# Optimization experiments

Hardware: AMD Instinct MI355X
Metric: run time of the kernel (lower is better)

## Reference

```python
import jax, jax.numpy as jnp
import numpy as np

EMB_DIM = 512          # hidden_dim d (complex dim); entity rows are 2*d
NUM_ENTITIES = 30000
GAMMA = 12.0
PHASE_RANGE = (GAMMA + 2.0) / EMB_DIM  # self.range in the torch module


def setup_inputs() -> dict:
    key = jax.random.key(0)
    k1, k2, k3, k4 = jax.random.split(key, 4)
    B = 8
    all_h = jax.random.randint(k1, (B,), 0, NUM_ENTITIES, dtype=jnp.int64 if jax.config.x64_enabled else jnp.int32)
    all_r = jax.random.randint(k2, (B,), 0, 1000, dtype=jnp.int64 if jax.config.x64_enabled else jnp.int32)
    eemb = jax.random.normal(k3, (NUM_ENTITIES, 2 * EMB_DIM), dtype=jnp.float32)
    remb = jax.random.normal(k4, (1000, EMB_DIM), dtype=jnp.float32)
    return {"all_h": all_h, "all_r": all_r, "eemb": eemb, "remb": remb}


def reference(all_h, all_r, eemb, remb):
    pi = 3.141592653589793
    # gather query embeddings
    h = eemb[all_h]                       # (B, 2d)
    re_h, im_h = jnp.split(h, 2, axis=-1)  # (B, d) each
    # project relation phases -> unit complex rotation
    phase = remb[all_r] / (PHASE_RANGE / pi)  # (B, d)
    re_r, im_r = jnp.cos(phase), jnp.sin(phase)
    # complex product h * r (rotation), once per query
    re_e = re_h * re_r - im_h * im_r      # (B, d)
    im_e = re_h * im_r + im_h * re_r      # (B, d)
    # distance to ALL entities: |h*r - t| summed over complex components
    re_t, im_t = jnp.split(eemb, 2, axis=-1)  # (N, d) each
    re_diff = re_e[:, None, :] - re_t[None, :, :]  # (B, N, d)
    im_diff = im_e[:, None, :] - im_t[None, :, :]  # (B, N, d)
    dist = jnp.sqrt(re_diff * re_diff + im_diff * im_diff).sum(axis=-1)  # (B, N)
    return GAMMA - dist
```

## Files before the change

### kernel.cpp

```cpp
#include <hip/hip_runtime.h>
#include <math.h>

#define EMB_DIM 512
#define N_Q 8
#define GAMMA_F 12.0f

typedef float f32x4 __attribute__((ext_vector_type(4)));

__global__ __launch_bounds__(256) void rotate_queries_kernel(
    const int* __restrict__ all_h,
    const int* __restrict__ all_r,
    const float* __restrict__ eemb,
    const float* __restrict__ remb,
    float* __restrict__ ws)
{
    const int p = blockIdx.x * 256 + threadIdx.x;
    const int b = p >> 9;
    const int j = p & (EMB_DIM - 1);
    const int h = all_h[b];
    const int r = all_r[b];
    const float SCALE = (float)(M_PI * (double)EMB_DIM / 14.0);
    float re_h = eemb[(size_t)h * (2 * EMB_DIM) + j];
    float im_h = eemb[(size_t)h * (2 * EMB_DIM) + EMB_DIM + j];
    float phase = remb[r * EMB_DIM + j] * SCALE;
    float s, c;
    __sincosf(phase, &s, &c);
    ws[p]                 = re_h * c - im_h * s;
    ws[N_Q * EMB_DIM + p] = re_h * s + im_h * c;
}

__global__ __launch_bounds__(256, 2) void rotate_score_kernel(
    const float* __restrict__ eemb,
    const float* __restrict__ ws,
    float* __restrict__ out,
    int N)
{
    const int lane  = threadIdx.x & 63;
    const int wid   = threadIdx.x >> 6;
    const int gwave = blockIdx.x * 4 + wid;
    const int nwav  = gridDim.x * 4;

    const int o0 = 4 * lane;
    const int o1 = 256 + 4 * lane;

    f32x4 qr0[N_Q], qr1[N_Q], qi0[N_Q], qi1[N_Q];
    #pragma unroll
    for (int b = 0; b < N_Q; ++b) {
        const float* re = ws + (b << 9);
        const float* im = re + N_Q * EMB_DIM;
        qr0[b] = *(const f32x4*)(re + o0);
        qr1[b] = *(const f32x4*)(re + o1);
        qi0[b] = *(const f32x4*)(im + o0);
        qi1[b] = *(const f32x4*)(im + o1);
    }

    int e = gwave;
    const float* rp = eemb + (size_t)e * (2 * EMB_DIM);
    f32x4 er0 = *(const f32x4*)(rp + o0);
    f32x4 er1 = *(const f32x4*)(rp + o1);
    f32x4 ei0 = *(const f32x4*)(rp + EMB_DIM + o0);
    f32x4 ei1 = *(const f32x4*)(rp + EMB_DIM + o1);

    for (; e < N; e += nwav) {
        int en = e + nwav;
        int ec = (en < N) ? en : 0;
        const float* np = eemb + (size_t)ec * (2 * EMB_DIM);
        f32x4 nr0 = *(const f32x4*)(np + o0);
        f32x4 nr1 = *(const f32x4*)(np + o1);
        f32x4 ni0 = *(const f32x4*)(np + EMB_DIM + o0);
        f32x4 ni1 = *(const f32x4*)(np + EMB_DIM + o1);

        float s[N_Q];
        #pragma unroll
        for (int b = 0; b < N_Q; ++b) {
            f32x4 dx = qr0[b] - er0;
            f32x4 dy = qi0[b] - ei0;
            f32x4 d2 = dx * dx + dy * dy;
            f32x4 ra;
            ra.x = __builtin_amdgcn_sqrtf(d2.x);
            ra.y = __builtin_amdgcn_sqrtf(d2.y);
            ra.z = __builtin_amdgcn_sqrtf(d2.z);
            ra.w = __builtin_amdgcn_sqrtf(d2.w);
            dx = qr1[b] - er1;
            dy = qi1[b] - ei1;
            d2 = dx * dx + dy * dy;
            f32x4 rb;
            rb.x = __builtin_amdgcn_sqrtf(d2.x);
            rb.y = __builtin_amdgcn_sqrtf(d2.y);
            rb.z = __builtin_amdgcn_sqrtf(d2.z);
            rb.w = __builtin_amdgcn_sqrtf(d2.w);
            f32x4 a = ra + rb;
            s[b] = (a.x + a.y) + (a.z + a.w);
        }

        const bool p1 = lane & 1;
        float u0, u1, u2, u3;
        {
            float x, z;
            x = p1 ? s[1] : s[0]; z = p1 ? s[0] : s[1]; u0 = x + __shfl_xor(z, 1);
            x = p1 ? s[3] : s[2]; z = p1 ? s[2] : s[3]; u1 = x + __shfl_xor(z, 1);
            x = p1 ? s[5] : s[4]; z = p1 ? s[4] : s[5]; u2 = x + __shfl_xor(z, 1);
            x = p1 ? s[7] : s[6]; z = p1 ? s[6] : s[7]; u3 = x + __shfl_xor(z, 1);
        }
        const bool p2 = lane & 2;
        float t0, t1;
        {
            float x, z;
            x = p2 ? u1 : u0; z = p2 ? u0 : u1; t0 = x + __shfl_xor(z, 2);
            x = p2 ? u3 : u2; z = p2 ? u2 : u3; t1 = x + __shfl_xor(z, 2);
        }
        const bool p3 = lane & 4;
        float u;
        {
            float x, z;
            x = p3 ? t1 : t0; z = p3 ? t0 : t1; u = x + __shfl_xor(z, 4);
        }
        u += __shfl_xor(u, 8);
        u += __shfl_xor(u, 16);
        u += __shfl_xor(u, 32);

        if (lane < N_Q) out[(size_t)lane * N + e] = GAMMA_F - u;

        er0 = nr0; er1 = nr1; ei0 = ni0; ei1 = ni1;
    }
}

extern "C" void kernel_launch(void* const* d_in, const int* in_sizes, int n_in,
                              void* d_out, int out_size, void* d_ws, size_t ws_size,
                              hipStream_t stream) {
    const int*   all_h = (const int*)d_in[0];
    const int*   all_r = (const int*)d_in[1];
    const float* eemb  = (const float*)d_in[2];
    const float* remb  = (const float*)d_in[3];
    float* out = (float*)d_out;
    float* ws  = (float*)d_ws;

    int N = in_sizes[2] / (2 * EMB_DIM);

    rotate_queries_kernel<<<16, 256, 0, stream>>>(all_h, all_r, eemb, remb, ws);

    rotate_score_kernel<<<512, 256, 0, stream>>>(eemb, ws, out, N);
}
```

Before: 184.8 us.

## Fuse query rotation into score kernel, split queries across waves, triple-buffer loads

Removes the separate query-rotation launch by having each wave compute its own rotated queries inline. Each wave now handles 4 of the 8 queries, so two waves share each entity row and the entity stream is read twice, but register pressure drops. This allows 3 blocks per CU and a larger grid of 768 blocks. The entity loads now use a three-deep rotating register buffer so loads run further ahead of the sqrt-heavy compute. The cost is doubled entity loads, which will mostly hit L2, plus redundant sincos work in every wave.

```diff
diff --git a/kernel.cpp b/kernel.cpp
--- a/kernel.cpp
+++ b/kernel.cpp
@@ -7,121 +7,137 @@
 
 typedef float f32x4 __attribute__((ext_vector_type(4)));
 
-__global__ __launch_bounds__(256) void rotate_queries_kernel(
+
+#define LOADE(R0, R1, I0, I1, EIDX)                                   \
+    do {                                                              \
+        int _ec = ((EIDX) < N) ? (EIDX) : 0;                          \
+        const float* _p = eemb + (size_t)_ec * (2 * EMB_DIM);         \
+        R0 = *(const f32x4*)(_p + o0);                                \
+        R1 = *(const f32x4*)(_p + o1);                                \
+        I0 = *(const f32x4*)(_p + EMB_DIM + o0);                      \
+        I1 = *(const f32x4*)(_p + EMB_DIM + o1);                      \
+    } while (0)
+
+#define SCORE(R0, R1, I0, I1, EIDX)                                   \
+    do {                                                              \
+        float s_[4];                                                  \
+        _Pragma("unroll")                                             \
+        for (int k = 0; k < 4; ++k) {                                 \
+            f32x4 dx = qr0[k] - R0;                                   \
+            f32x4 dy = qi0[k] - I0;                                   \
+            f32x4 d2 = dx * dx + dy * dy;                             \
+            f32x4 ra;                                                 \
+            ra.x = __builtin_amdgcn_sqrtf(d2.x);                      \
+            ra.y = __builtin_amdgcn_sqrtf(d2.y);                      \
+            ra.z = __builtin_amdgcn_sqrtf(d2.z);                      \
+            ra.w = __builtin_amdgcn_sqrtf(d2.w);                      \
+            dx = qr1[k] - R1;                                         \
+            dy = qi1[k] - I1;                                         \
+            d2 = dx * dx + dy * dy;                                   \
+            f32x4 rb;                                                 \
+            rb.x = __builtin_amdgcn_sqrtf(d2.x);                      \
+            rb.y = __builtin_amdgcn_sqrtf(d2.y);                      \
+            rb.z = __builtin_amdgcn_sqrtf(d2.z);                      \
+            rb.w = __builtin_amdgcn_sqrtf(d2.w);                      \
+            f32x4 a = ra + rb;                                        \
+            s_[k] = (a.x + a.y) + (a.z + a.w);                        \
+        }                                                             \
+        const bool p1 = lane & 1;                                     \
+        float x_, z_, u0, u1;                                         \
+        x_ = p1 ? s_[1] : s_[0]; z_ = p1 ? s_[0] : s_[1];             \
+        u0 = x_ + __shfl_xor(z_, 1);                                  \
+        x_ = p1 ? s_[3] : s_[2]; z_ = p1 ? s_[2] : s_[3];             \
+        u1 = x_ + __shfl_xor(z_, 1);                                  \
+        const bool p2 = lane & 2;                                     \
+        x_ = p2 ? u1 : u0; z_ = p2 ? u0 : u1;                         \
+        float u = x_ + __shfl_xor(z_, 2);                             \
+        u += __shfl_xor(u, 4);                                        \
+        u += __shfl_xor(u, 8);                                        \
+        u += __shfl_xor(u, 16);                                       \
+        u += __shfl_xor(u, 32);                                       \
+        if (lane < 4 && (EIDX) < N)                                   \
+            out[(size_t)(qh * 4 + lane) * N + (EIDX)] = GAMMA_F - u;  \
+    } while (0)
+
+__global__ __launch_bounds__(256, 3) void rotate_score_kernel(
     const int* __restrict__ all_h,
     const int* __restrict__ all_r,
     const float* __restrict__ eemb,
     const float* __restrict__ remb,
-    float* __restrict__ ws)
-{
-    const int p = blockIdx.x * 256 + threadIdx.x;
-    const int b = p >> 9;
-    const int j = p & (EMB_DIM - 1);
-    const int h = all_h[b];
-    const int r = all_r[b];
-    const float SCALE = (float)(M_PI * (double)EMB_DIM / 14.0);
-    float re_h = eemb[(size_t)h * (2 * EMB_DIM) + j];
-    float im_h = eemb[(size_t)h * (2 * EMB_DIM) + EMB_DIM + j];
-    float phase = remb[r * EMB_DIM + j] * SCALE;
-    float s, c;
-    __sincosf(phase, &s, &c);
-    ws[p]                 = re_h * c - im_h * s;
-    ws[N_Q * EMB_DIM + p] = re_h * s + im_h * c;
-}
-
-__global__ __launch_bounds__(256, 2) void rotate_score_kernel(
-    const float* __restrict__ eemb,
-    const float* __restrict__ ws,
     float* __restrict__ out,
     int N)
 {
     const int lane  = threadIdx.x & 63;
     const int wid   = threadIdx.x >> 6;
     const int gwave = blockIdx.x * 4 + wid;
-    const int nwav  = gridDim.x * 4;
+    const int W     = gridDim.x * 4;
+    const int qh    = gwave & 1;
+    const int e0    = gwave >> 1;
+    const int estep = W >> 1;
 
     const int o0 = 4 * lane;
     const int o1 = 256 + 4 * lane;
 
-    f32x4 qr0[N_Q], qr1[N_Q], qi0[N_Q], qi1[N_Q];
-    #pragma unroll
-    for (int b = 0; b < N_Q; ++b) {
-        const float* re = ws + (b << 9);
-        const float* im = re + N_Q * EMB_DIM;
-        qr0[b] = *(const f32x4*)(re + o0);
-        qr1[b] = *(const f32x4*)(re + o1);
-        qi0[b] = *(const f32x4*)(im + o0);
-        qi1[b] = *(const f32x4*)(im + o1);
+    f32x4 qr0[4], qr1[4], qi0[4], qi1[4];
+    {
+        const float SCALE = (float)(M_PI * (double)EMB_DIM / 14.0);
+        #pragma unroll
+        for (int k = 0; k < 4; ++k) {
+            int q = qh * 4 + k;
+            int h = all_h[q];
+            int r = all_r[q];
+            const float* hp = eemb + (size_t)h * (2 * EMB_DIM);
+            const float* rp = remb + (size_t)r * EMB_DIM;
+            f32x4 reh0 = *(const f32x4*)(hp + o0);
+            f32x4 reh1 = *(const f32x4*)(hp + o1);
+            f32x4 imh0 = *(const f32x4*)(hp + EMB_DIM + o0);
+            f32x4 imh1 = *(const f32x4*)(hp + EMB_DIM + o1);
+            f32x4 ph0  = *(const f32x4*)(rp + o0);
+            f32x4 ph1  = *(const f32x4*)(rp + o1);
+            f32x4 s0, c0, s1, c1;
+            #pragma unroll
+            for (int j = 0; j < 4; ++j) {
+                float s, c;
+                __sincosf(ph0[j] * SCALE, &s, &c);
+                s0[j] = s; c0[j] = c;
+                __sincosf(ph1[j] * SCALE, &s, &c);
+                s1[j] = s; c1[j] = c;
+            }
+            qr0[k] = reh0 * c0 - imh0 * s0;
+            qr1[k] = reh1 * c1 - imh1 * s1;
+            qi0[k] = reh0 * s0 + imh0 * c0;
+            qi1[k] = reh1 * s1 + imh1 * c1;
+        }
     }
 
-    int e = gwave;
-    const float* rp = eemb + (size_t)e * (2 * EMB_DIM);
-    f32x4 er0 = *(const f32x4*)(rp + o0);
-    f32x4 er1 = *(const f32x4*)(rp + o1);
-    f32x4 ei0 = *(const f32x4*)(rp + EMB_DIM + o0);
-    f32x4 ei1 = *(const f32x4*)(rp + EMB_DIM + o1);
+    f32x4 Ar0, Ar1, Ai0, Ai1;
+    f32x4 Br0, Br1, Bi0, Bi1;
+    f32x4 Cr0, Cr1, Ci0, Ci1;
 
-    for (; e < N; e += nwav) {
-        int en = e + nwav;
-        int ec = (en < N) ? en : 0;
-        const float* np = eemb + (size_t)ec * (2 * EMB_DIM);
-        f32x4 nr0 = *(const f32x4*)(np + o0);
-        f32x4 nr1 = *(const f32x4*)(np + o1);
-        f32x4 ni0 = *(const f32x4*)(np + EMB_DIM + o0);
-        f32x4 ni1 = *(const f32x4*)(np + EMB_DIM + o1);
+    const int itmax = (N + estep - 1) / estep;
+    int e = e0;
+    LOADE(Ar0, Ar1, Ai0, Ai1, e);
+    LOADE(Br0, Br1, Bi0, Bi1, e + estep);
 
-        float s[N_Q];
-        #pragma unroll
-        for (int b = 0; b < N_Q; ++b) {
-            f32x4 dx = qr0[b] - er0;
-            f32x4 dy = qi0[b] - ei0;
-            f32x4 d2 = dx * dx + dy * dy;
-            f32x4 ra;
-            ra.x = __builtin_amdgcn_sqrtf(d2.x);
-            ra.y = __builtin_amdgcn_sqrtf(d2.y);
-            ra.z = __builtin_amdgcn_sqrtf(d2.z);
-            ra.w = __builtin_amdgcn_sqrtf(d2.w);
-            dx = qr1[b] - er1;
-            dy = qi1[b] - ei1;
-            d2 = dx * dx + dy * dy;
-            f32x4 rb;
-            rb.x = __builtin_amdgcn_sqrtf(d2.x);
-            rb.y = __builtin_amdgcn_sqrtf(d2.y);
-            rb.z = __builtin_amdgcn_sqrtf(d2.z);
-            rb.w = __builtin_amdgcn_sqrtf(d2.w);
-            f32x4 a = ra + rb;
-            s[b] = (a.x + a.y) + (a.z + a.w);
-        }
-
-        const bool p1 = lane & 1;
-        float u0, u1, u2, u3;
-        {
-            float x, z;
-            x = p1 ? s[1] : s[0]; z = p1 ? s[0] : s[1]; u0 = x + __shfl_xor(z, 1);
-            x = p1 ? s[3] : s[2]; z = p1 ? s[2] : s[3]; u1 = x + __shfl_xor(z, 1);
-            x = p1 ? s[5] : s[4]; z = p1 ? s[4] : s[5]; u2 = x + __shfl_xor(z, 1);
-            x = p1 ? s[7] : s[6]; z = p1 ? s[6] : s[7]; u3 = x + __shfl_xor(z, 1);
-        }
-        const bool p2 = lane & 2;
-        float t0, t1;
-        {
-            float x, z;
-            x = p2 ? u1 : u0; z = p2 ? u0 : u1; t0 = x + __shfl_xor(z, 2);
-            x = p2 ? u3 : u2; z = p2 ? u2 : u3; t1 = x + __shfl_xor(z, 2);
-        }
-        const bool p3 = lane & 4;
-        float u;
-        {
-            float x, z;
-            x = p3 ? t1 : t0; z = p3 ? t0 : t1; u = x + __shfl_xor(z, 4);
-        }
-        u += __shfl_xor(u, 8);
-        u += __shfl_xor(u, 16);
-        u += __shfl_xor(u, 32);
-
-        if (lane < N_Q) out[(size_t)lane * N + e] = GAMMA_F - u;
-
-        er0 = nr0; er1 = nr1; ei0 = ni0; ei1 = ni1;
+    int it = 0;
+    for (; it + 3 <= itmax; it += 3) {
+        LOADE(Cr0, Cr1, Ci0, Ci1, e + 2 * estep);
+        SCORE(Ar0, Ar1, Ai0, Ai1, e);
+        e += estep;
+        LOADE(Ar0, Ar1, Ai0, Ai1, e + 2 * estep);
+        SCORE(Br0, Br1, Bi0, Bi1, e);
+        e += estep;
+        LOADE(Br0, Br1, Bi0, Bi1, e + 2 * estep);
+        SCORE(Cr0, Cr1, Ci0, Ci1, e);
+        e += estep;
+    }
+    if (it < itmax) {
+        SCORE(Ar0, Ar1, Ai0, Ai1, e);
+        e += estep;
+        ++it;
+    }
+    if (it < itmax) {
+        SCORE(Br0, Br1, Bi0, Bi1, e);
     }
 }
 
@@ -133,11 +149,8 @@
     const float* eemb  = (const float*)d_in[2];
     const float* remb  = (const float*)d_in[3];
     float* out = (float*)d_out;
-    float* ws  = (float*)d_ws;
 
     int N = in_sizes[2] / (2 * EMB_DIM);
 
-    rotate_queries_kernel<<<16, 256, 0, stream>>>(all_h, all_r, eemb, remb, ws);
-
-    rotate_score_kernel<<<512, 256, 0, stream>>>(eemb, ws, out, N);
+    rotate_score_kernel<<<768, 256, 0, stream>>>(all_h, all_r, eemb, remb, out, N);
 }
```

Measured after the change: 188.0 us. No clear change (+1.7%).
